# Kernel optimization log

Hardware: AMD Instinct MI355X
Metric: run time of the kernel (lower is better)

Reference implementation:

```python
import jax, jax.numpy as jnp
import numpy as np

LMAX = 5
RESOLUTION = 12
ASPECT_RATIO = 2
BATCH = 256
NB = 2 * RESOLUTION                       # res_beta = 24
NA = round(2 * ASPECT_RATIO * RESOLUTION)  # res_alpha = res_gamma = 48
DIM = sum((2 * l + 1) ** 2 for l in range(LMAX + 1))  # 286

# normalize2mom constant for tanh: (E_{z~N(0,1)}[tanh(z)^2])^{-1/2}
_x = np.linspace(-12.0, 12.0, 1_000_001)
_pdf = np.exp(-0.5 * _x * _x) / np.sqrt(2.0 * np.pi)
ACT_CST = float(np.trapz(np.tanh(_x) ** 2 * _pdf, _x) ** -0.5)  # ~1.5927


def _su2_generators(j):
    m = np.arange(-j, j)
    raising = np.diag(-np.sqrt(j * (j + 1) - m * (m + 1)), k=-1).astype(complex)
    m = np.arange(-j + 1, j + 1)
    lowering = np.diag(np.sqrt(j * (j + 1) - m * (m - 1)), k=1).astype(complex)
    m = np.arange(-j, j + 1)
    return np.stack([0.5 * (raising + lowering), np.diag(1j * m), -0.5j * (raising - lowering)])


def _q_real_to_complex(l):
    q = np.zeros((2 * l + 1, 2 * l + 1), dtype=complex)
    for m in range(-l, 0):
        q[l + m, l + abs(m)] = 1 / np.sqrt(2)
        q[l + m, l - abs(m)] = -1j / np.sqrt(2)
    q[l, l] = 1
    for m in range(1, l + 1):
        q[l + m, l + abs(m)] = (-1) ** m / np.sqrt(2)
        q[l + m, l - abs(m)] = 1j * (-1) ** m / np.sqrt(2)
    return (-1j) ** l * q


def _so3_generators(l):
    X = _su2_generators(l)
    Q = _q_real_to_complex(l)
    return np.real(np.conj(Q.T)[None] @ X @ Q[None])  # real [3, 2l+1, 2l+1]


def _expm_angles(A, t):
    """exp(t_n * A) for real antisymmetric A via eigendecomposition. -> [n, d, d] real"""
    vals, vecs = np.linalg.eig(A.astype(complex))
    inv = np.linalg.inv(vecs)
    phases = np.exp(t[:, None] * vals[None, :])  # [n, d]
    return np.real(np.einsum('ij,nj,jk->nik', vecs, phases, inv))


def _build_D_and_qw():
    # Euler angle grids (e3nn SO3Grid convention)
    b = (np.arange(NB) + 0.5) / NB * np.pi          # beta   [nb]
    a = np.arange(NA) / NA * 2.0 * np.pi            # alpha=gamma [na]
    blocks = []
    for l in range(LMAX + 1):
        X = _so3_generators(l)
        Ra = _expm_angles(X[1], a)   # exp(alpha * X1)  [na,d,d]
        Rb = _expm_angles(X[0], b)   # exp(beta  * X0)  [nb,d,d]
        # D^l(a,b,c) = Ra[a] @ Rb[b] @ Ra[c]
        Dl = np.einsum('xij,yjk,zkl->xyzil', Ra, Rb, Ra)
        blocks.append(np.sqrt(2 * l + 1) * Dl.reshape(NA, NB, NA, -1))
    D = np.concatenate(blocks, axis=-1).astype(np.float32)  # [na, nb, na, dim]
    # lie_learn / Kostelec-Rockmore quadrature weights for beta
    bb = NB // 2
    k = np.arange(bb)
    j = np.arange(2 * bb)
    w = (2.0 / bb) * np.sin(np.pi * (2 * j + 1) / (4.0 * bb)) * np.sum(
        (1.0 / (2 * k + 1))[None, :]
        * np.sin((2 * j[:, None] + 1) * (2 * k[None, :] + 1) * np.pi / (4.0 * bb)),
        axis=1,
    )
    w = w / (2.0 * (2 * bb) ** 2)
    qw = (w * NB ** 2 / NA ** 2).astype(np.float32)  # [nb]
    return jnp.asarray(D), jnp.asarray(qw)


def setup_inputs() -> dict:
    key = jax.random.key(0)
    features = jax.random.normal(key, (BATCH, DIM), dtype=jnp.float32)
    D, qw = _build_D_and_qw()
    return {"features": features, "D": D, "qw": qw}


def reference(features, D, qw):
    dim = D.shape[-1]
    s = jnp.sqrt(jnp.asarray(dim, features.dtype))
    # to_grid: [B, dim] x [na, nb, na, dim] -> [B, na, nb, na]
    g = jnp.einsum('bi,xyzi->bxyz', features, D) / s
    # normalized pointwise nonlinearity on SO(3) samples
    g = ACT_CST * jnp.tanh(g)
    # from_grid: quadrature-weighted projection back onto flat Wigner basis
    return jnp.einsum('bxyz,y,xyzi->bi', g, qw, D) * s
```

## Files before the change

kernel.cpp:

```cpp
#include <hip/hip_runtime.h>
#include <hip/hip_bf16.h>

#define DIM    286
#define DIMP   288
#define NBATCH 256
#define NB_    24
#define NA_    48
#define ZC     32
#define NTILES 1728
#define NCHUNK 256
#define S_CONST 16.911534525287763f
#define INV_S   0.05913123959890826f
#define ACT_CST 1.5927f
#define TWO_LOG2E 2.8853900817779268f

typedef short bf16x8 __attribute__((ext_vector_type(8)));
typedef float f32x4  __attribute__((ext_vector_type(4)));

#define WS_FBF  0u
#define WS_PART 147456u

typedef const __attribute__((address_space(1))) char GA;
typedef __attribute__((address_space(3))) char LA;
__device__ __forceinline__ void gload_lds16(const void* g, void* l) {
    __builtin_amdgcn_global_load_lds((GA*)g, (LA*)l, 16, 0, 0);
}

__global__ void k_prepF(const float* __restrict__ F, __hip_bfloat16* __restrict__ Fbf) {
    int o = blockIdx.x * 256 + threadIdx.x;
    int row = o / DIMP, col = o % DIMP;
    float v = (col < DIM) ? F[row * DIM + col] * INV_S : 0.f;
    Fbf[o] = __float2bfloat16(v);
}

__launch_bounds__(512, 2)
__global__ void k_main(const __hip_bfloat16* __restrict__ Fbf,
                       const float* __restrict__ D,
                       const float* __restrict__ qw,
                       __hip_bfloat16* __restrict__ part) {
    __shared__ __align__(16) float Traw[2][9216];
    __shared__ __align__(16) char DsB[18432];
    __shared__ __align__(16) char DtB[18432];
    __shared__ __align__(16) char GsB[16384];
    __shared__ float qs[24];

    int t = threadIdx.x;
    int wave = t >> 6, lane = t & 63, ln = lane & 15, q = lane >> 4;
    int cA = (ln * 64 + q * 16) ^ ((ln & 7) << 4);
    int rq = ln * 64 + q * 16;
    int gA0 = (wave << 11) + (rq ^ ((ln >> 2) << 4));
    int gA1 = (wave << 11) + 1024 + (rq ^ ((4 + (ln >> 2)) << 4));

    if (t < 24) qs[t] = qw[t] * S_CONST;

    int rowbase = wave * 32;
    const __hip_bfloat16* fp0 = Fbf + (size_t)(rowbase + ln) * DIMP + q * 8;
    const __hip_bfloat16* fp1 = fp0 + 16 * DIMP;

    f32x4 acc[2][18];
    #pragma unroll
    for (int h = 0; h < 2; ++h)
        #pragma unroll
        for (int n = 0; n < 18; ++n) acc[h][n] = (f32x4){0.f, 0.f, 0.f, 0.f};

    int bx = blockIdx.x;
    int tstart = (bx < 192) ? bx * 7 : bx * 6 + 192;
    int ntile = (bx < 192) ? 7 : 6;

    #define STAGE(TI, BUF) do {                                                    \
        const char* _s = (const char*)(D + (size_t)(tstart + (TI)) * 9152);        \
        char* _d = (char*)Traw[BUF];                                               \
        _Pragma("unroll")                                                          \
        for (int _j = 0; _j < 5; ++_j) {                                           \
            int _c = wave + _j * 8;                                                \
            if (_c < 35 || (_c == 35 && lane < 48))                                \
                gload_lds16(_s + _c * 1024 + lane * 16, _d + _c * 1024);           \
        }                                                                          \
    } while (0)

    STAGE(0, 0);
    STAGE(1, 1);

    #pragma unroll 1
    for (int k = 0; k < ntile; ++k) {
        if (k + 1 < ntile) {
            if (wave < 4) asm volatile("s_waitcnt vmcnt(5)" ::: "memory");
            else          asm volatile("s_waitcnt vmcnt(4)" ::: "memory");
        } else {
            asm volatile("s_waitcnt vmcnt(0)" ::: "memory");
        }
        __builtin_amdgcn_s_barrier();

        const float* T = Traw[k & 1];
        int z0 = (tstart + k) * 32;
        #pragma unroll
        for (int m = 0; m < 9; ++m) {
            int d = t + m * 512;
            int z = d / 144, i2 = d % 144;
            int i = i2 * 2;
            __hip_bfloat162 o2;
            if (i < DIM) {
                float2 v = *(const float2*)(&T[z * DIM + i]);
                o2.x = __float2bfloat16(v.x); o2.y = __float2bfloat16(v.y);
            } else {
                o2.x = __float2bfloat16(0.f); o2.y = o2.x;
            }
            int off = (((i >> 5) * 2048) + z * 64 + (i & 31) * 2) ^ ((z & 7) << 4);
            *(__hip_bfloat162*)(DsB + off) = o2;
        }
        #pragma unroll
        for (int s = 0; s < 3; ++s) {
            int idx = t + s * 512;
            if (idx < 1152) {
                int i = idx >> 2, zc = idx & 3;
                __hip_bfloat16 o8[8];
                #pragma unroll
                for (int j = 0; j < 8; ++j) {
                    int zl = zc * 8 + j;
                    int y = ((z0 + zl) / NA_) % NB_;
                    o8[j] = __float2bfloat16(T[zl * DIM + i] * qs[y]);
                }
                int off = (i * 64 + zc * 16) ^ ((i & 7) << 4);
                *(bf16x8*)(DtB + off) = *(const bf16x8*)o8;
            }
        }
        asm volatile("s_waitcnt lgkmcnt(0)" ::: "memory");
        __builtin_amdgcn_s_barrier();

        if (k + 2 < ntile) STAGE(k + 2, k & 1);

        f32x4 g00 = (f32x4){0.f,0.f,0.f,0.f}, g01 = (f32x4){0.f,0.f,0.f,0.f};
        f32x4 g10 = (f32x4){0.f,0.f,0.f,0.f}, g11 = (f32x4){0.f,0.f,0.f,0.f};
        #pragma unroll 3
        for (int ks = 0; ks < 9; ++ks) {
            bf16x8 a0 = *(const bf16x8*)(fp0 + ks * 32);
            bf16x8 a1 = *(const bf16x8*)(fp1 + ks * 32);
            bf16x8 b0 = *(const bf16x8*)(DsB + ks * 2048 + cA);
            bf16x8 b1 = *(const bf16x8*)(DsB + ks * 2048 + 1024 + cA);
            g00 = __builtin_amdgcn_mfma_f32_16x16x32_bf16(a0, b0, g00, 0, 0, 0);
            g01 = __builtin_amdgcn_mfma_f32_16x16x32_bf16(a0, b1, g01, 0, 0, 0);
            g10 = __builtin_amdgcn_mfma_f32_16x16x32_bf16(a1, b0, g10, 0, 0, 0);
            g11 = __builtin_amdgcn_mfma_f32_16x16x32_bf16(a1, b1, g11, 0, 0, 0);
        }
        #pragma unroll
        for (int h = 0; h < 2; ++h) {
            #pragma unroll
            for (int zh = 0; zh < 2; ++zh) {
                f32x4 g = (h == 0) ? (zh == 0 ? g00 : g01) : (zh == 0 ? g10 : g11);
                #pragma unroll
                for (int r = 0; r < 4; ++r) {
                    float x = g[r];
                    float a = fabsf(x);
                    float e = __builtin_amdgcn_exp2f(-TWO_LOG2E * a);
                    float v = ACT_CST - 2.f * ACT_CST * e * __builtin_amdgcn_rcpf(1.f + e);
                    v = copysignf(v, x);
                    int row = h * 16 + q * 4 + r;
                    int goff = (wave << 11)
                             + ((row * 64 + (zh * 16 + ln) * 2) ^ ((row >> 2) << 4));
                    *(__hip_bfloat16*)(GsB + goff) = __float2bfloat16(v);
                }
            }
        }
        bf16x8 a20 = *(const bf16x8*)(GsB + gA0);
        bf16x8 a21 = *(const bf16x8*)(GsB + gA1);
        #pragma unroll
        for (int nf = 0; nf < 18; ++nf) {
            bf16x8 b2 = *(const bf16x8*)(DtB + nf * 1024 + cA);
            acc[0][nf] = __builtin_amdgcn_mfma_f32_16x16x32_bf16(a20, b2, acc[0][nf], 0, 0, 0);
            acc[1][nf] = __builtin_amdgcn_mfma_f32_16x16x32_bf16(a21, b2, acc[1][nf], 0, 0, 0);
        }
        __builtin_amdgcn_s_barrier();
    }
    #undef STAGE

    __hip_bfloat16* pw = part + (size_t)bx * (NBATCH * DIMP) + (size_t)rowbase * DIMP;
    #pragma unroll
    for (int h = 0; h < 2; ++h) {
        #pragma unroll
        for (int m = 0; m < 9; ++m) {
            __hip_bfloat16 o8[8];
            #pragma unroll
            for (int j = 0; j < 8; ++j)
                o8[j] = __float2bfloat16(acc[h][2 * m + (j >> 2)][j & 3]);
            *(bf16x8*)(pw + (size_t)((h * 9 + m) * 64 + lane) * 8) = *(const bf16x8*)o8;
        }
    }
}

__global__ void k_reduce(const __hip_bfloat16* __restrict__ part, float* __restrict__ out) {
    __shared__ float red[3][16][8];
    int t = threadIdx.x, wave = t >> 6, lane = t & 63;
    int j = lane & 15;
    int zg = wave * 4 + (lane >> 4);
    int s = blockIdx.x * 16 + j;
    const __hip_bfloat16* p = part + (size_t)s * 8;
    float sum[8];
    #pragma unroll
    for (int kk = 0; kk < 8; ++kk) sum[kk] = 0.f;
    #pragma unroll 4
    for (int ii = 0; ii < 16; ++ii) {
        bf16x8 v = *(const bf16x8*)(p + (size_t)(zg * 16 + ii) * (NBATCH * DIMP));
        #pragma unroll
        for (int kk = 0; kk < 8; ++kk) {
            __hip_bfloat16 h; *(short*)&h = v[kk];
            sum[kk] += __bfloat162float(h);
        }
    }
    #pragma unroll
    for (int kk = 0; kk < 8; ++kk) {
        sum[kk] += __shfl_down(sum[kk], 16);
        sum[kk] += __shfl_down(sum[kk], 32);
    }
    if (wave > 0 && lane < 16) {
        #pragma unroll
        for (int kk = 0; kk < 8; ++kk) red[wave - 1][lane][kk] = sum[kk];
    }
    __syncthreads();
    if (wave == 0 && lane < 16) {
        #pragma unroll
        for (int w = 0; w < 3; ++w)
            #pragma unroll
            for (int kk = 0; kk < 8; ++kk) sum[kk] += red[w][lane][kk];
        int wr = s / 1152, si = s % 1152;
        int lane_m = si % 64, m9 = si / 64;
        int h = m9 / 9, m = m9 % 9, q = lane_m >> 4, ln = lane_m & 15;
        int rowb = wr * 32 + h * 16 + q * 4;
        #pragma unroll
        for (int j8 = 0; j8 < 8; ++j8) {
            int nf = 2 * m + (j8 >> 2), r = j8 & 3;
            int i = nf * 16 + ln;
            if (i < DIM) out[(rowb + r) * DIM + i] = sum[j8];
        }
    }
}

extern "C" void kernel_launch(void* const* d_in, const int* in_sizes, int n_in,
                              void* d_out, int out_size, void* d_ws, size_t ws_size,
                              hipStream_t stream) {
    const float* F  = (const float*)d_in[0];
    const float* D  = (const float*)d_in[1];
    const float* qw = (const float*)d_in[2];
    char* ws = (char*)d_ws;
    __hip_bfloat16* Fbf = (__hip_bfloat16*)(ws + WS_FBF);
    __hip_bfloat16* part = (__hip_bfloat16*)(ws + WS_PART);

    k_prepF<<<288, 256, 0, stream>>>(F, Fbf);
    k_main<<<NCHUNK, 512, 0, stream>>>(Fbf, D, qw, part);
    k_reduce<<<576, 256, 0, stream>>>(part, (float*)d_out);
}
```

Measured before the change: 139.9 us.

## Split batch across two blocks per tile chunk and single-buffer D staging

Blocks shrink from 512 to 256 threads, and a second grid dimension splits the 256 batch rows into two halves of 128. Each block now stages and converts every D tile itself, so global D traffic and bf16 conversion work are doubled. The stage buffer drops from double to single buffering to cut LDS use, which permits more resident blocks but removes the two-deep prefetch overlap. The hidden epilogue must also index partials by blockIdx.y, and that part is not visible.

Result: slower. 173.4 us (+24.0%).

```diff
diff --git a/kernel.cpp b/kernel.cpp
--- a/kernel.cpp
+++ b/kernel.cpp
@@ -33,16 +33,16 @@
     Fbf[o] = __float2bfloat16(v);
 }
 
-__launch_bounds__(512, 2)
+__launch_bounds__(256, 2)
 __global__ void k_main(const __hip_bfloat16* __restrict__ Fbf,
                        const float* __restrict__ D,
                        const float* __restrict__ qw,
                        __hip_bfloat16* __restrict__ part) {
-    __shared__ __align__(16) float Traw[2][9216];
+    __shared__ __align__(16) float Traw[9216];
     __shared__ __align__(16) char DsB[18432];
     __shared__ __align__(16) char DtB[18432];
-    __shared__ __align__(16) char GsB[16384];
-    __shared__ float qs[24];
+    __shared__ __align__(16) char GsB[8192];
+    float* qs = &Traw[9152];
 
     int t = threadIdx.x;
     int wave = t >> 6, lane = t & 63, ln = lane & 15, q = lane >> 4;
@@ -53,7 +53,7 @@
 
     if (t < 24) qs[t] = qw[t] * S_CONST;
 
-    int rowbase = wave * 32;
+    int rowbase = blockIdx.y * 128 + wave * 32;
     const __hip_bfloat16* fp0 = Fbf + (size_t)(rowbase + ln) * DIMP + q * 8;
     const __hip_bfloat16* fp1 = fp0 + 16 * DIMP;
 
@@ -67,40 +67,33 @@
     int tstart = (bx < 192) ? bx * 7 : bx * 6 + 192;
     int ntile = (bx < 192) ? 7 : 6;
 
-    #define STAGE(TI, BUF) do {                                                    \
+    #define STAGE(TI) do {                                                         \
         const char* _s = (const char*)(D + (size_t)(tstart + (TI)) * 9152);        \
-        char* _d = (char*)Traw[BUF];                                               \
+        char* _d = (char*)Traw;                                                    \
         _Pragma("unroll")                                                          \
-        for (int _j = 0; _j < 5; ++_j) {                                           \
-            int _c = wave + _j * 8;                                                \
+        for (int _j = 0; _j < 9; ++_j) {                                           \
+            int _c = wave + _j * 4;                                                \
             if (_c < 35 || (_c == 35 && lane < 48))                                \
                 gload_lds16(_s + _c * 1024 + lane * 16, _d + _c * 1024);           \
         }                                                                          \
     } while (0)
 
-    STAGE(0, 0);
-    STAGE(1, 1);
+    STAGE(0);
 
     #pragma unroll 1
     for (int k = 0; k < ntile; ++k) {
-        if (k + 1 < ntile) {
-            if (wave < 4) asm volatile("s_waitcnt vmcnt(5)" ::: "memory");
-            else          asm volatile("s_waitcnt vmcnt(4)" ::: "memory");
-        } else {
-            asm volatile("s_waitcnt vmcnt(0)" ::: "memory");
-        }
+        asm volatile("s_waitcnt vmcnt(0)" ::: "memory");
         __builtin_amdgcn_s_barrier();
 
-        const float* T = Traw[k & 1];
-        int z0 = (tstart + k) * 32;
-        #pragma unroll
-        for (int m = 0; m < 9; ++m) {
-            int d = t + m * 512;
+        int z0t = (tstart + k) * 32;
+        #pragma unroll
+        for (int m = 0; m < 18; ++m) {
+            int d = t + m * 256;
             int z = d / 144, i2 = d % 144;
             int i = i2 * 2;
             __hip_bfloat162 o2;
             if (i < DIM) {
-                float2 v = *(const float2*)(&T[z * DIM + i]);
+                float2 v = *(const float2*)(&Traw[z * DIM + i]);
                 o2.x = __float2bfloat16(v.x); o2.y = __float2bfloat16(v.y);
             } else {
                 o2.x = __float2bfloat16(0.f); o2.y = o2.x;
@@ -109,16 +102,16 @@
             *(__hip_bfloat162*)(DsB + off) = o2;
         }
         #pragma unroll
-        for (int s = 0; s < 3; ++s) {
-            int idx = t + s * 512;
+        for (int s5 = 0; s5 < 5; ++s5) {
+            int idx = t + s5 * 256;
             if (idx < 1152) {
                 int i = idx >> 2, zc = idx & 3;
                 __hip_bfloat16 o8[8];
                 #pragma unroll
                 for (int j = 0; j < 8; ++j) {
                     int zl = zc * 8 + j;
-                    int y = ((z0 + zl) / NA_) % NB_;
-                    o8[j] = __float2bfloat16(T[zl * DIM + i] * qs[y]);
+                    int y = ((z0t + zl) / NA_) % NB_;
+                    o8[j] = __float2bfloat16(Traw[zl * DIM + i] * qs[y]);
                 }
                 int off = (i * 64 + zc * 16) ^ ((i & 7) << 4);
                 *(bf16x8*)(DtB + off) = *(const bf16x8*)o8;
@@ -127,7 +120,7 @@
         asm volatile("s_waitcnt lgkmcnt(0)" ::: "memory");
         __builtin_amdgcn_s_barrier();
 
-        if (k + 2 < ntile) STAGE(k + 2, k & 1);
+        if (k + 1 < ntile) STAGE(k + 1);
 
         f32x4 g00 = (f32x4){0.f,0.f,0.f,0.f}, g01 = (f32x4){0.f,0.f,0.f,0.f};
         f32x4 g10 = (f32x4){0.f,0.f,0.f,0.f}, g11 = (f32x4){0.f,0.f,0.f,0.f};
@@ -245,6 +238,6 @@
     __hip_bfloat16* part = (__hip_bfloat16*)(ws + WS_PART);
 
     k_prepF<<<288, 256, 0, stream>>>(F, Fbf);
-    k_main<<<NCHUNK, 512, 0, stream>>>(Fbf, D, qw, part);
+    k_main<<<dim3(NCHUNK, 2), 256, 0, stream>>>(Fbf, D, qw, part);
     k_reduce<<<576, 256, 0, stream>>>(part, (float*)d_out);
 }
```
